# Kernel tuning notes

Hardware: AMD Instinct MI355X
Metric: run time of the kernel (lower is better)

## Reference

```python
import jax, jax.numpy as jnp
import numpy as np

B, S = 4, 1024          # 4 prefill sequences of length 1024 (cu_seqlens equal-length)
D_MODEL = 2048
N_HEADS = 32
N_KV_HEADS = 8
HEAD_DIM = D_MODEL // N_HEADS          # 64
GROUPS = N_HEADS // N_KV_HEADS         # 4
ROPE_THETA = 10000.0
SCALE = HEAD_DIM ** -0.5


def setup_inputs() -> dict:
    key = jax.random.key(0)
    ks = jax.random.split(key, 6)
    T = B * S
    hidden_states = jax.random.normal(ks[0], (T, D_MODEL), jnp.float32)
    # rotary tables: positions restart per sequence (prefill)
    pos = jnp.tile(jnp.arange(S, dtype=jnp.float32), B)            # [T]
    inv_freq = 1.0 / (ROPE_THETA ** (jnp.arange(0, HEAD_DIM, 2, dtype=jnp.float32) / HEAD_DIM))
    freqs = pos[:, None] * inv_freq[None, :]                        # [T, HEAD_DIM/2]
    cos, sin = jnp.cos(freqs), jnp.sin(freqs)
    std = D_MODEL ** -0.5
    Wq = jax.random.normal(ks[1], (D_MODEL, N_HEADS * HEAD_DIM), jnp.float32) * std
    Wk = jax.random.normal(ks[2], (D_MODEL, N_KV_HEADS * HEAD_DIM), jnp.float32) * std
    Wv = jax.random.normal(ks[3], (D_MODEL, N_KV_HEADS * HEAD_DIM), jnp.float32) * std
    Wo = jax.random.normal(ks[4], (N_HEADS * HEAD_DIM, D_MODEL), jnp.float32) * std
    return {"hidden_states": hidden_states, "cos": cos, "sin": sin,
            "Wq": Wq, "Wk": Wk, "Wv": Wv, "Wo": Wo}


def _rope(x, cos, sin):
    # NeoX-style rotary: x [T, H, D], cos/sin [T, D/2]
    half = x.shape[-1] // 2
    x1, x2 = x[..., :half], x[..., half:]
    c, s = cos[:, None, :], sin[:, None, :]
    return jnp.concatenate([x1 * c - x2 * s, x2 * c + x1 * s], axis=-1)


def reference(hidden_states, cos, sin, Wq, Wk, Wv, Wo):
    T = hidden_states.shape[0]
    q = (hidden_states @ Wq).reshape(T, N_HEADS, HEAD_DIM)
    k = (hidden_states @ Wk).reshape(T, N_KV_HEADS, HEAD_DIM)
    v = (hidden_states @ Wv).reshape(T, N_KV_HEADS, HEAD_DIM)
    q = _rope(q, cos, sin)
    k = _rope(k, cos, sin)
    # equal-length varlen prefill -> [B, S, H, D]
    q = q.reshape(B, S, N_HEADS, HEAD_DIM)
    k = jnp.repeat(k.reshape(B, S, N_KV_HEADS, HEAD_DIM), GROUPS, axis=2)  # GQA expand
    v = jnp.repeat(v.reshape(B, S, N_KV_HEADS, HEAD_DIM), GROUPS, axis=2)
    scores = jnp.einsum("bqhd,bkhd->bhqk", q, k) * SCALE
    causal = jnp.tril(jnp.ones((S, S), dtype=bool))
    scores = jnp.where(causal[None, None], scores, jnp.finfo(scores.dtype).min)
    probs = jax.nn.softmax(scores, axis=-1)
    attn = jnp.einsum("bhqk,bkhd->bqhd", probs, v).reshape(T, N_HEADS * HEAD_DIM)
    return attn @ Wo
```

## Files before the change

### kernel.cpp

```cpp
#include <hip/hip_runtime.h>
#include <type_traits>


typedef __bf16 bf16x8 __attribute__((ext_vector_type(8)));
typedef __bf16 bf16x4 __attribute__((ext_vector_type(4)));
typedef float f32x4 __attribute__((ext_vector_type(4)));
typedef unsigned short u16;
typedef unsigned int u32;

#define DEVI __device__ __forceinline__

DEVI u16 f2bf(float f) {
  u32 u = __builtin_bit_cast(u32, f);
  u += 0x7FFF + ((u >> 16) & 1);
  return (u16)(u >> 16);
}

DEVI void ld16_lds(const void* g, void* l) {
  __builtin_amdgcn_global_load_lds((const __attribute__((address_space(1))) u32*)g,
                                   (__attribute__((address_space(3))) u32*)l, 16, 0, 0);
}

template <int N> DEVI void waitvm() {
  if constexpr (N == 0) asm volatile("s_waitcnt vmcnt(0)" ::: "memory");
  else if constexpr (N == 8) asm volatile("s_waitcnt vmcnt(8)" ::: "memory");
  else if constexpr (N == 10) asm volatile("s_waitcnt vmcnt(10)" ::: "memory");
  else static_assert(N == 0, "unsupported vmcnt");
}
template <int N> DEVI void lgkmN() {
  if constexpr (N == 0) asm volatile("s_waitcnt lgkmcnt(0)" ::: "memory");
  else if constexpr (N == 4) asm volatile("s_waitcnt lgkmcnt(4)" ::: "memory");
  else if constexpr (N == 6) asm volatile("s_waitcnt lgkmcnt(6)" ::: "memory");
  else static_assert(N == 0, "unsupported lgkmcnt");
  __builtin_amdgcn_sched_barrier(0);
}
DEVI void barrier() { __builtin_amdgcn_s_barrier(); }

__global__ __launch_bounds__(256) void prep(const float* __restrict__ hs, u16* __restrict__ hsB,
                                            const float* __restrict__ Wq, const float* __restrict__ Wk,
                                            const float* __restrict__ Wv, const float* __restrict__ Wo,
                                            u16* __restrict__ wqkvT, u16* __restrict__ woT,
                                            float qscale) {
  int b = blockIdx.x;
  if (b < 2048) {
    const int t0 = b * 256 + threadIdx.x;
#pragma unroll
    for (int k = 0; k < 4; ++k) {
      int i = t0 + k * 524288;
      float4 v = ((const float4*)hs)[i];
      ushort4 o;
      o.x = f2bf(v.x); o.y = f2bf(v.y); o.z = f2bf(v.z); o.w = f2bf(v.w);
      ((ushort4*)hsB)[i] = o;
    }
    return;
  }
  b -= 2048;
  const float* src; u16* dst; int R, C, bx, by; float sc = 1.0f;
  if (b < 1024)      { src = Wq; dst = wqkvT;                         R = 2048; C = 2048; bx = b & 31; by = b >> 5; sc = qscale; }
  else if (b < 1280) { b -= 1024; src = Wk; dst = wqkvT + (size_t)2048 * 2048; R = 2048; C = 512; bx = b & 7; by = b >> 3; }
  else if (b < 1536) { b -= 1280; src = Wv; dst = wqkvT + (size_t)2560 * 2048; R = 2048; C = 512; bx = b & 7; by = b >> 3; }
  else               { b -= 1536; src = Wo; dst = woT;                R = 2048; C = 2048; bx = b & 31; by = b >> 5; }
  __shared__ float tile[64][65];
  const int c0 = bx * 64, r0 = by * 64;
  {
    const int tx = (threadIdx.x & 15) * 4, ty = threadIdx.x >> 4;
#pragma unroll
    for (int i = 0; i < 4; ++i) {
      int row = ty + 16 * i;
      float4 v = *(const float4*)&src[(size_t)(r0 + row) * C + c0 + tx];
      tile[row][tx] = v.x; tile[row][tx + 1] = v.y;
      tile[row][tx + 2] = v.z; tile[row][tx + 3] = v.w;
    }
  }
  __syncthreads();
  {
    const int ox = threadIdx.x & 63, oy = threadIdx.x >> 6;
#pragma unroll
    for (int k = 0; k < 16; ++k) {
      int j = oy + 4 * k;
      dst[(size_t)(c0 + j) * R + r0 + ox] = f2bf(tile[ox][j] * sc);
    }
  }
}

template <typename OutT, int BN>
__global__ __launch_bounds__(256, 2) void gemm6(const u16* __restrict__ A,
                                                const u16* __restrict__ BT,
                                                OutT* __restrict__ C, int M, int N, int K) {
  constexpr int NF = BN / 32;
  constexpr int NH = NF / 2;
  constexpr int HW = BN / 2;
  constexpr int SW = HW / 2;
  constexpr int LB0 = BN / 64;
  constexpr int VMW = 4 + 2 * LB0;
  __shared__ u16 As[2][128 * 64];
  __shared__ u16 Bs[2][BN * 64];
  const int tid = threadIdx.x;
  const int lane = tid & 63, wave = tid >> 6;
  const int quad = lane >> 4, l16 = lane & 15;

  const int nwg = gridDim.x * gridDim.y;
  const int bid = blockIdx.y * gridDim.x + blockIdx.x;
  const int swz = (bid & 7) * (nwg >> 3) + (bid >> 3);
  const int m0 = (swz / gridDim.x) * 128, n0 = (swz % gridDim.x) * BN;
  const int wr = wave >> 1, wc = wave & 1;

  f32x4 acc[4][NF] = {};

  auto stage = [&](int t, u16* Ad, u16* Bd) {
    {
      const u16* G = A + (size_t)m0 * K + t * 64;
#pragma unroll
      for (int i = 0; i < 4; ++i) {
        int id = i * 256 + tid, row = id >> 3, ch = id & 7;
        ld16_lds(G + (size_t)row * K + (ch ^ (row & 7)) * 8, Ad + id * 8);
      }
    }
#pragma unroll
    for (int h = 0; h < 2; ++h) {
      const u16* G = BT + (size_t)(n0 + h * HW) * K + t * 64;
#pragma unroll
      for (int i = 0; i < LB0; ++i) {
        int id = i * 256 + tid, row = id >> 3, ch = id & 7;
        ld16_lds(G + (size_t)row * K + (ch ^ (row & 7)) * 8, Bd + (h * HW * 64) + id * 8);
      }
    }
  };

  bf16x8 af[4][2], b0[NH][2], b1[NH][2];
  auto ldAF = [&](const u16* Ab) {
#pragma unroll
    for (int i = 0; i < 4; ++i)
#pragma unroll
      for (int ks = 0; ks < 2; ++ks) {
        int r = wr * 64 + i * 16 + l16;
        af[i][ks] = *(const bf16x8*)&Ab[r * 64 + (((ks * 4 + quad) ^ (r & 7)) * 8)];
      }
  };
  auto ldB = [&](bf16x8 (&bv)[NH][2], int half, const u16* Bb) {
#pragma unroll
    for (int j = 0; j < NH; ++j)
#pragma unroll
      for (int ks = 0; ks < 2; ++ks) {
        int rb = half * HW + wc * SW + j * 16 + l16;
        bv[j][ks] = *(const bf16x8*)&Bb[rb * 64 + (((ks * 4 + quad) ^ (rb & 7)) * 8)];
      }
  };
  auto mmh = [&](const bf16x8 (&bv)[NH][2], int jo) {
    __builtin_amdgcn_s_setprio(1);
#pragma unroll
    for (int i = 0; i < 4; ++i)
#pragma unroll
      for (int j = 0; j < NH; ++j)
#pragma unroll
        for (int ks = 0; ks < 2; ++ks)
          acc[i][jo + j] =
              __builtin_amdgcn_mfma_f32_16x16x32_bf16(af[i][ks], bv[j][ks], acc[i][jo + j], 0, 0, 0);
    __builtin_amdgcn_s_setprio(0);
  };

  const int NT = K / 64;

  stage(0, As[0], Bs[0]);
  stage(1, As[1], Bs[1]);
  waitvm<VMW>();
  barrier();

#pragma unroll 2
  for (int t = 0; t < NT; ++t) {
    const int buf = t & 1;
    ldB(b0, 0, Bs[buf]);
    __builtin_amdgcn_sched_barrier(0);
    ldAF(As[buf]);
    __builtin_amdgcn_sched_barrier(0);
    ldB(b1, 1, Bs[buf]);
    lgkmN<2 * NH>();
    mmh(b0, 0);
    lgkmN<0>();
    barrier();
    if (t + 2 < NT) stage(t + 2, As[buf], Bs[buf]);
    mmh(b1, NH);
    if (t + 1 < NT) {
      if (t + 2 < NT) waitvm<VMW>();
      else waitvm<0>();
      barrier();
    }
  }

#pragma unroll
  for (int i = 0; i < 4; ++i) {
    int row = m0 + wr * 64 + i * 16 + quad * 4;
#pragma unroll
    for (int j = 0; j < NF; ++j) {
      int half = j / NH, jj = j % NH;
      int col = n0 + half * HW + wc * SW + jj * 16 + l16;
#pragma unroll
      for (int r = 0; r < 4; ++r) {
        size_t off = (size_t)(row + r) * N + col;
        if constexpr (sizeof(OutT) == 2) C[off] = f2bf(acc[i][j][r]);
        else C[off] = acc[i][j][r];
      }
    }
  }
}

__global__ __launch_bounds__(256) void kv_prep(u16* __restrict__ qkv,
                                               u16* __restrict__ vkt,
                                               const float* __restrict__ cs,
                                               const float* __restrict__ sn) {
  const int kt = blockIdx.x, kvh = blockIdx.y, b = blockIdx.z;
  const int tid = threadIdx.x;
  const size_t tok0 = (size_t)b * 1024 + (size_t)kt * 128;

  {
    const int r = tid >> 1, hf = tid & 1;
    const size_t t = tok0 + r;
    const float* cr = cs + t * 32;
    const float* sr = sn + t * 32;
    u16* krow = qkv + t * 3072 + 2048 + kvh * 64;
#pragma unroll
    for (int gg = 0; gg < 2; ++gg) {
      const int g = hf * 2 + gg;
      bf16x8 a = *(bf16x8*)&krow[g * 8];
      bf16x8 b2 = *(bf16x8*)&krow[g * 8 + 32];
#pragma unroll
      for (int e = 0; e < 8; ++e) {
        float cv = cr[g * 8 + e], sv = sr[g * 8 + e];
        float x1 = (float)a[e], x2 = (float)b2[e];
        a[e] = (__bf16)(x1 * cv - x2 * sv);
        b2[e] = (__bf16)(x2 * cv + x1 * sv);
      }
      *(bf16x8*)&krow[g * 8] = a;
      *(bf16x8*)&krow[g * 8 + 32] = b2;
    }
  }

  __shared__ u16 Vn[128 * 64];
  const u16* src = qkv + tok0 * 3072 + 2560 + kvh * 64;
  {
    int tok = tid >> 1, hf = tid & 1;
    const uint4* s4 = (const uint4*)(src + (size_t)tok * 3072 + hf * 32);
    uint4* d4 = (uint4*)&Vn[tok * 64 + hf * 32];
#pragma unroll
    for (int j = 0; j < 4; j++) d4[j] = s4[j];
  }
  __syncthreads();
  u16* img = vkt + ((((size_t)b * 8 + kvh) * 8 + kt) << 13);
#pragma unroll
  for (int i = 0; i < 4; i++) {
    int c = tid * 4 + i;
    int dd = c >> 4, chsw = c & 15;
    int ch = chsw ^ (dd & 15);
    u16 tmp[8];
#pragma unroll
    for (int p = 0; p < 8; p++) {
      int col = ch * 8 + p;
      int g = col >> 5, kl = col & 31;
      int kph = ((kl >> 2) & 1) * 16 + ((kl >> 4) & 1) * 8 + ((kl >> 3) & 1) * 4 + (kl & 3);
      tmp[p] = Vn[(g * 32 + kph) * 64 + dd];
    }
    *(uint4*)&img[c * 8] = *(const uint4*)tmp;
  }
}

__global__ __launch_bounds__(256, 2) void flash_attn(const u16* __restrict__ qkv,
                                                     const u16* __restrict__ vkt,
                                                     u16* __restrict__ attn,
                                                     const float* __restrict__ cs,
                                                     const float* __restrict__ sn) {
  __shared__ u16 Ks[2][128 * 64];
  __shared__ u16 VT[2][64 * 128];

  const int tid = threadIdx.x;
  const int lane = tid & 63, wave = tid >> 6;
  const int quad = lane >> 4, l16 = lane & 15;
  const int qtA = blockIdx.x, qtB = 7 - blockIdx.x;
  const int h = blockIdx.y, b = blockIdx.z, kvh = h >> 2;
  const size_t tokBase = (size_t)b * 1024;
  const int qcol = h * 64, kcol = 2048 + kvh * 64;
  const int srow = tid >> 3, spc = tid & 7, ssc = spc ^ (srow & 7);

  auto stageK = [&](const u16* gbase, u16* L) {
#pragma unroll
    for (int i = 0; i < 4; i++)
      ld16_lds(gbase + (size_t)(srow + i * 32) * 3072 + ssc * 8, &L[tid * 8 + i * 2048]);
  };
  const u16* vimg = vkt + (((size_t)b * 8 + kvh) << 16);
  auto stageV = [&](int kt, u16* L) {
    const u16* g = vimg + ((size_t)kt << 13);
#pragma unroll
    for (int i = 0; i < 4; i++)
      ld16_lds(g + i * 2048 + tid * 8, &L[tid * 8 + i * 2048]);
  };

  stageK(qkv + (tokBase + qtA * 128) * 3072 + qcol, Ks[0]);
  stageK(qkv + (tokBase + qtB * 128) * 3072 + qcol, Ks[1]);
  __syncthreads();

  {
    const int r = tid >> 1, hf = tid & 1;
#pragma unroll
    for (int qt = 0; qt < 2; ++qt) {
      u16* L = (qt == 0) ? Ks[0] : Ks[1];
      const size_t t = tokBase + (size_t)((qt == 0) ? qtA : qtB) * 128 + r;
      const float* cr = cs + t * 32;
      const float* sr = sn + t * 32;
#pragma unroll
      for (int gg = 0; gg < 2; ++gg) {
        const int g = hf * 2 + gg;
        const int c1 = g ^ (r & 7);
        const int c2 = (g + 4) ^ (r & 7);
        bf16x8 a = *(bf16x8*)&L[r * 64 + c1 * 8];
        bf16x8 b2 = *(bf16x8*)&L[r * 64 + c2 * 8];
#pragma unroll
        for (int e = 0; e < 8; ++e) {
          float cv = cr[g * 8 + e], sv = sr[g * 8 + e];
          float x1 = (float)a[e], x2 = (float)b2[e];
          a[e] = (__bf16)(x1 * cv - x2 * sv);
          b2[e] = (__bf16)(x2 * cv + x1 * sv);
        }
        *(bf16x8*)&L[r * 64 + c1 * 8] = a;
        *(bf16x8*)&L[r * 64 + c2 * 8] = b2;
      }
    }
  }
  __syncthreads();

  bf16x8 qfA[2][2], qfB[2][2];
#pragma unroll
  for (int nq = 0; nq < 2; nq++) {
    int qrow = wave * 32 + nq * 16 + l16;
#pragma unroll
    for (int ks = 0; ks < 2; ks++) {
      int c = (ks * 4 + quad) ^ (qrow & 7);
      qfA[nq][ks] = *(const bf16x8*)&Ks[0][qrow * 64 + c * 8];
      qfB[nq][ks] = *(const bf16x8*)&Ks[1][qrow * 64 + c * 8];
    }
  }
  __syncthreads();

  float lA[2] = {0.f, 0.f}, lB[2] = {0.f, 0.f};
  f32x4 oA[4][2] = {}, oB[4][2] = {};

  auto proc = [&](const bf16x8 (&kf)[2][2], const bf16x8 (&va)[4], const bf16x8 (&qf)[2][2],
                  f32x4 (&o)[4][2], float (&lacc)[2], bool msk, int c) {
    f32x4 s[2][2] = {};
    __builtin_amdgcn_s_setprio(1);
#pragma unroll
    for (int mkl = 0; mkl < 2; mkl++)
#pragma unroll
      for (int ks = 0; ks < 2; ks++) {
        s[0][mkl] = __builtin_amdgcn_mfma_f32_16x16x32_bf16(kf[mkl][ks], qf[0][ks], s[0][mkl], 0, 0, 0);
        s[1][mkl] = __builtin_amdgcn_mfma_f32_16x16x32_bf16(kf[mkl][ks], qf[1][ks], s[1][mkl], 0, 0, 0);
      }
    __builtin_amdgcn_s_setprio(0);
    if (msk) {
#pragma unroll
      for (int nq = 0; nq < 2; nq++) {
        int q = wave * 32 + nq * 16 + l16;
#pragma unroll
        for (int mkl = 0; mkl < 2; mkl++)
#pragma unroll
          for (int r = 0; r < 4; r++)
            if ((c * 2 + mkl) * 16 + quad * 4 + r > q) s[nq][mkl][r] = -3e38f;
      }
    }
    bf16x8 pf[2];
#pragma unroll
    for (int nq = 0; nq < 2; nq++) {
      float a0 = 0.f;
#pragma unroll
      for (int mkl = 0; mkl < 2; mkl++)
#pragma unroll
        for (int r = 0; r < 4; r++) {
          float p = __builtin_amdgcn_exp2f(s[nq][mkl][r]);
          s[nq][mkl][r] = p;
          a0 += p;
        }
      lacc[nq] += a0;
      pf[nq][0] = (__bf16)s[nq][0][0]; pf[nq][1] = (__bf16)s[nq][0][1];
      pf[nq][2] = (__bf16)s[nq][0][2]; pf[nq][3] = (__bf16)s[nq][0][3];
      pf[nq][4] = (__bf16)s[nq][1][0]; pf[nq][5] = (__bf16)s[nq][1][1];
      pf[nq][6] = (__bf16)s[nq][1][2]; pf[nq][7] = (__bf16)s[nq][1][3];
    }
    __builtin_amdgcn_s_setprio(1);
#pragma unroll
    for (int md = 0; md < 4; md++) {
      o[md][0] = __builtin_amdgcn_mfma_f32_16x16x32_bf16(va[md], pf[0], o[md][0], 0, 0, 0);
      o[md][1] = __builtin_amdgcn_mfma_f32_16x16x32_bf16(va[md], pf[1], o[md][1], 0, 0, 0);
    }
    __builtin_amdgcn_s_setprio(0);
  };

  stageK(qkv + tokBase * 3072 + kcol, Ks[0]);
  stageV(0, VT[0]);

  for (int kt = 0; kt <= qtB; kt++) {
    const int cur = kt & 1;
    __syncthreads();
    if (kt < qtB) {
      stageK(qkv + (tokBase + (kt + 1) * 128) * 3072 + kcol, Ks[1 - cur]);
      stageV(kt + 1, VT[1 - cur]);
    }
    const bool doA = (kt <= qtA), mA = (kt == qtA), mB = (kt == qtB);
    const u16* K = Ks[cur];
    const u16* V = VT[cur];
#pragma unroll
    for (int c = 0; c < 4; c++) {
      bf16x8 kf[2][2];
#pragma unroll
      for (int mkl = 0; mkl < 2; mkl++) {
        int krow = (c * 2 + mkl) * 16 + l16;
#pragma unroll
        for (int ks = 0; ks < 2; ks++)
          kf[mkl][ks] = *(const bf16x8*)&K[krow * 64 + ((ks * 4 + quad) ^ (krow & 7)) * 8];
      }
      bf16x8 va[4];
#pragma unroll
      for (int md = 0; md < 4; md++) {
        int dd = md * 16 + l16;
        va[md] = *(const bf16x8*)&V[dd * 128 + ((c * 4 + quad) ^ l16) * 8];
      }
      proc(kf, va, qfB, oB, lB, mB, c);
      if (doA) proc(kf, va, qfA, oA, lA, mA, c);
    }
  }

  auto epilogue = [&](const f32x4 (&o)[4][2], const float (&lacc)[2], int qt_tile) {
#pragma unroll
    for (int nq = 0; nq < 2; nq++) {
      float l = lacc[nq];
      l += __shfl_xor(l, 16);
      l += __shfl_xor(l, 32);
      float inv = 1.0f / l;
      int t = qt_tile * 128 + wave * 32 + nq * 16 + l16;
      size_t rowOff = (tokBase + t) * 2048 + qcol;
#pragma unroll
      for (int md = 0; md < 4; md++) {
        bf16x4 w;
        w[0] = (__bf16)(o[md][nq][0] * inv);
        w[1] = (__bf16)(o[md][nq][1] * inv);
        w[2] = (__bf16)(o[md][nq][2] * inv);
        w[3] = (__bf16)(o[md][nq][3] * inv);
        *(bf16x4*)&attn[rowOff + md * 16 + quad * 4] = w;
      }
    }
  };
  epilogue(oB, lB, qtB);
  epilogue(oA, lA, qtA);
}

extern "C" void kernel_launch(void* const* d_in, const int* in_sizes, int n_in,
                              void* d_out, int out_size, void* d_ws, size_t ws_size,
                              hipStream_t stream) {
  const float* hs = (const float*)d_in[0];
  const float* cs = (const float*)d_in[1];
  const float* sn = (const float*)d_in[2];
  const float* Wq = (const float*)d_in[3];
  const float* Wk = (const float*)d_in[4];
  const float* Wv = (const float*)d_in[5];
  const float* Wo = (const float*)d_in[6];
  float* out = (float*)d_out;

  char* ws = (char*)d_ws;
  u16* hsB   = (u16*)(ws);
  u16* vkt   = (u16*)(ws);
  u16* wqkvT = (u16*)(ws + 16777216);
  u16* woT   = (u16*)(ws + 29360128);
  u16* qkv   = (u16*)(ws + 37748736);
  u16* attnB = (u16*)(ws + 62914560);

  const float QSCALE = 0.18033688011112042f;

  prep<<<4608, 256, 0, stream>>>(hs, hsB, Wq, Wk, Wv, Wo, wqkvT, woT, QSCALE);

  gemm6<u16, 192><<<dim3(16, 32), 256, 0, stream>>>(hsB, wqkvT, qkv, 4096, 3072, 2048);
  kv_prep<<<dim3(8, 8, 4), 256, 0, stream>>>(qkv, vkt, cs, sn);
  flash_attn<<<dim3(4, 32, 4), 256, 0, stream>>>(qkv, vkt, attnB, cs, sn);
  gemm6<float, 128><<<dim3(16, 32), 256, 0, stream>>>(attnB, woT, out, 4096, 2048, 2048);
}
```

Measured before the change: 238.0 us.

## Restructure GEMM into 8-wave 256-row tiles with phased interleaved staging

```diff
diff --git a/kernel.cpp b/kernel.cpp
--- a/kernel.cpp
+++ b/kernel.cpp
@@ -23,15 +23,12 @@
 
 template <int N> DEVI void waitvm() {
   if constexpr (N == 0) asm volatile("s_waitcnt vmcnt(0)" ::: "memory");
-  else if constexpr (N == 8) asm volatile("s_waitcnt vmcnt(8)" ::: "memory");
-  else if constexpr (N == 10) asm volatile("s_waitcnt vmcnt(10)" ::: "memory");
+  else if constexpr (N == 6) asm volatile("s_waitcnt vmcnt(6)" ::: "memory");
+  else if constexpr (N == 7) asm volatile("s_waitcnt vmcnt(7)" ::: "memory");
   else static_assert(N == 0, "unsupported vmcnt");
 }
-template <int N> DEVI void lgkmN() {
-  if constexpr (N == 0) asm volatile("s_waitcnt lgkmcnt(0)" ::: "memory");
-  else if constexpr (N == 4) asm volatile("s_waitcnt lgkmcnt(4)" ::: "memory");
-  else if constexpr (N == 6) asm volatile("s_waitcnt lgkmcnt(6)" ::: "memory");
-  else static_assert(N == 0, "unsupported lgkmcnt");
+DEVI void lgkm0() {
+  asm volatile("s_waitcnt lgkmcnt(0)" ::: "memory");
   __builtin_amdgcn_sched_barrier(0);
 }
 DEVI void barrier() { __builtin_amdgcn_s_barrier(); }
@@ -84,16 +81,13 @@
 }
 
 template <typename OutT, int BN>
-__global__ __launch_bounds__(256, 2) void gemm6(const u16* __restrict__ A,
+__global__ __launch_bounds__(512, 1) void gemm7(const u16* __restrict__ A,
                                                 const u16* __restrict__ BT,
                                                 OutT* __restrict__ C, int M, int N, int K) {
-  constexpr int NF = BN / 32;
-  constexpr int NH = NF / 2;
-  constexpr int HW = BN / 2;
-  constexpr int SW = HW / 2;
-  constexpr int LB0 = BN / 64;
-  constexpr int VMW = 4 + 2 * LB0;
-  __shared__ u16 As[2][128 * 64];
+  constexpr int NH = BN / 64;
+  constexpr int LBB = BN / 64;
+  constexpr int NST = 4 + LBB;
+  __shared__ u16 As[2][256 * 64];
   __shared__ u16 Bs[2][BN * 64];
   const int tid = threadIdx.x;
   const int lane = tid & 63, wave = tid >> 6;
@@ -102,98 +96,97 @@
   const int nwg = gridDim.x * gridDim.y;
   const int bid = blockIdx.y * gridDim.x + blockIdx.x;
   const int swz = (bid & 7) * (nwg >> 3) + (bid >> 3);
-  const int m0 = (swz / gridDim.x) * 128, n0 = (swz % gridDim.x) * BN;
-  const int wr = wave >> 1, wc = wave & 1;
-
-  f32x4 acc[4][NF] = {};
-
-  auto stage = [&](int t, u16* Ad, u16* Bd) {
-    {
+  const int m0 = (swz / gridDim.x) * 256, n0 = (swz % gridDim.x) * BN;
+  const int wm = wave >> 1, wn = wave & 1;
+
+  f32x4 acc[4][2 * NH] = {};
+
+  auto stage = [&](int t, int u) {
+    u16* Ad = &As[t & 1][0];
+    u16* Bd = &Bs[t & 1][0];
+    if (u < 2) {
       const u16* G = A + (size_t)m0 * K + t * 64;
 #pragma unroll
-      for (int i = 0; i < 4; ++i) {
-        int id = i * 256 + tid, row = id >> 3, ch = id & 7;
+      for (int i = 0; i < 2; ++i) {
+        int id = (u * 2 + i) * 512 + tid, row = id >> 3, ch = id & 7;
         ld16_lds(G + (size_t)row * K + (ch ^ (row & 7)) * 8, Ad + id * 8);
       }
-    }
-#pragma unroll
-    for (int h = 0; h < 2; ++h) {
-      const u16* G = BT + (size_t)(n0 + h * HW) * K + t * 64;
-#pragma unroll
-      for (int i = 0; i < LB0; ++i) {
-        int id = i * 256 + tid, row = id >> 3, ch = id & 7;
-        ld16_lds(G + (size_t)row * K + (ch ^ (row & 7)) * 8, Bd + (h * HW * 64) + id * 8);
-      }
-    }
-  };
-
-  bf16x8 af[4][2], b0[NH][2], b1[NH][2];
-  auto ldAF = [&](const u16* Ab) {
+    } else {
+      const u16* G = BT + (size_t)n0 * K + t * 64;
+#pragma unroll
+      for (int i = 0; i < LBB; ++i) {
+        int id = i * 512 + tid, row = id >> 3, ch = id & 7;
+        ld16_lds(G + (size_t)row * K + (ch ^ (row & 7)) * 8, Bd + id * 8);
+      }
+    }
+  };
+
+  bf16x8 af[4], bf[NH];
+  auto ldA = [&](int ks, const u16* Ab) {
+#pragma unroll
+    for (int i = 0; i < 4; ++i) {
+      int r = wm * 64 + i * 16 + l16;
+      af[i] = *(const bf16x8*)&Ab[r * 64 + (((ks * 4 + quad) ^ (r & 7)) * 8)];
+    }
+  };
+  auto ldBf = [&](int nh, int ks, const u16* Bb) {
+#pragma unroll
+    for (int j = 0; j < NH; ++j) {
+      int rb = wn * (BN / 2) + (nh * NH + j) * 16 + l16;
+      bf[j] = *(const bf16x8*)&Bb[rb * 64 + (((ks * 4 + quad) ^ (rb & 7)) * 8)];
+    }
+  };
+  auto mm = [&](int nh) {
+    __builtin_amdgcn_s_setprio(1);
 #pragma unroll
     for (int i = 0; i < 4; ++i)
 #pragma unroll
-      for (int ks = 0; ks < 2; ++ks) {
-        int r = wr * 64 + i * 16 + l16;
-        af[i][ks] = *(const bf16x8*)&Ab[r * 64 + (((ks * 4 + quad) ^ (r & 7)) * 8)];
-      }
-  };
-  auto ldB = [&](bf16x8 (&bv)[NH][2], int half, const u16* Bb) {
-#pragma unroll
-    for (int j = 0; j < NH; ++j)
-#pragma unroll
-      for (int ks = 0; ks < 2; ++ks) {
-        int rb = half * HW + wc * SW + j * 16 + l16;
-        bv[j][ks] = *(const bf16x8*)&Bb[rb * 64 + (((ks * 4 + quad) ^ (rb & 7)) * 8)];
-      }
-  };
-  auto mmh = [&](const bf16x8 (&bv)[NH][2], int jo) {
-    __builtin_amdgcn_s_setprio(1);
-#pragma unroll
-    for (int i = 0; i < 4; ++i)
-#pragma unroll
       for (int j = 0; j < NH; ++j)
-#pragma unroll
-        for (int ks = 0; ks < 2; ++ks)
-          acc[i][jo + j] =
-              __builtin_amdgcn_mfma_f32_16x16x32_bf16(af[i][ks], bv[j][ks], acc[i][jo + j], 0, 0, 0);
+        acc[i][nh * NH + j] =
+            __builtin_amdgcn_mfma_f32_16x16x32_bf16(af[i], bf[j], acc[i][nh * NH + j], 0, 0, 0);
     __builtin_amdgcn_s_setprio(0);
   };
 
   const int NT = K / 64;
 
-  stage(0, As[0], Bs[0]);
-  stage(1, As[1], Bs[1]);
-  waitvm<VMW>();
+  stage(0, 0); stage(0, 1); stage(0, 2);
+  stage(1, 0); stage(1, 1); stage(1, 2);
+  waitvm<NST>();
   barrier();
 
-#pragma unroll 2
+#pragma unroll 1
   for (int t = 0; t < NT; ++t) {
-    const int buf = t & 1;
-    ldB(b0, 0, Bs[buf]);
-    __builtin_amdgcn_sched_barrier(0);
-    ldAF(As[buf]);
-    __builtin_amdgcn_sched_barrier(0);
-    ldB(b1, 1, Bs[buf]);
-    lgkmN<2 * NH>();
-    mmh(b0, 0);
-    lgkmN<0>();
+    const u16* Ab = &As[t & 1][0];
+    const u16* Bb = &Bs[t & 1][0];
+    const bool st = (t >= 1 && t + 1 < NT);
+    ldA(0, Ab); ldBf(0, 0, Bb);
+    if (st) stage(t + 1, 0);
+    barrier(); lgkm0();
+    mm(0);
     barrier();
-    if (t + 2 < NT) stage(t + 2, As[buf], Bs[buf]);
-    mmh(b1, NH);
-    if (t + 1 < NT) {
-      if (t + 2 < NT) waitvm<VMW>();
-      else waitvm<0>();
-      barrier();
-    }
+    ldBf(1, 0, Bb);
+    if (st) stage(t + 1, 1);
+    barrier(); lgkm0();
+    mm(1);
+    barrier();
+    ldA(1, Ab); ldBf(0, 1, Bb);
+    if (st) stage(t + 1, 2);
+    barrier(); lgkm0();
+    mm(0);
+    barrier();
+    ldBf(1, 1, Bb);
+    barrier(); lgkm0();
+    mm(1);
+    waitvm<0>();
+    barrier();
   }
 
 #pragma unroll
   for (int i = 0; i < 4; ++i) {
-    int row = m0 + wr * 64 + i * 16 + quad * 4;
-#pragma unroll
-    for (int j = 0; j < NF; ++j) {
-      int half = j / NH, jj = j % NH;
-      int col = n0 + half * HW + wc * SW + jj * 16 + l16;
+    int row = m0 + wm * 64 + i * 16 + quad * 4;
+#pragma unroll
+    for (int j = 0; j < 2 * NH; ++j) {
+      int col = n0 + wn * (BN / 2) + j * 16 + l16;
 #pragma unroll
       for (int r = 0; r < 4; ++r) {
         size_t off = (size_t)(row + r) * N + col;
@@ -474,8 +467,8 @@
 
   prep<<<4608, 256, 0, stream>>>(hs, hsB, Wq, Wk, Wv, Wo, wqkvT, woT, QSCALE);
 
-  gemm6<u16, 192><<<dim3(16, 32), 256, 0, stream>>>(hsB, wqkvT, qkv, 4096, 3072, 2048);
+  gemm7<u16, 192><<<dim3(16, 16), 512, 0, stream>>>(hsB, wqkvT, qkv, 4096, 3072, 2048);
   kv_prep<<<dim3(8, 8, 4), 256, 0, stream>>>(qkv, vkt, cs, sn);
   flash_attn<<<dim3(4, 32, 4), 256, 0, stream>>>(qkv, vkt, attnB, cs, sn);
-  gemm6<float, 128><<<dim3(16, 32), 256, 0, stream>>>(attnB, woT, out, 4096, 2048, 2048);
-}
+  gemm7<float, 128><<<dim3(16, 16), 512, 0, stream>>>(attnB, woT, out, 4096, 2048, 2048);
+}
```

Result: slower. 266.7 us (+12.1%).
